# Performance work log

Measured on AMD Instinct MI355X. Metric: run time of the kernel, lower is better.

## Reference

```python
import jax, jax.numpy as jnp
import numpy as np

B, T, D, H, E, O, A = 8192, 223, 7, 128, 50, 29, 9
IMPUTE_W, LABEL_W = 0.3, 1.0

def setup_inputs() -> dict:
    key = jax.random.key(0)
    ks = jax.random.split(key, 32)
    u = lambda k, shape, fan: jax.random.uniform(k, shape, jnp.float32, -1.0/np.sqrt(fan), 1.0/np.sqrt(fan))
    return {
        'values':    jax.random.normal(ks[0], (B, T, D), jnp.float32),
        'masks':     (jax.random.uniform(ks[1], (B, T, D)) < 0.8).astype(jnp.float32),
        'deltas':    jax.random.uniform(ks[2], (B, T, D), jnp.float32) * 5.0,
        'probs':     jax.nn.softmax(jax.random.normal(ks[3], (B, O), jnp.float32), axis=1),
        'ancillary': jax.random.normal(ks[4], (B, A), jnp.float32),
        'labels':    jax.random.randint(ks[5], (B,), 0, O, jnp.int32),
        'W_td_h': u(ks[6], (H, D), H),  'b_td_h': u(ks[7], (H,), H),
        'W_td_x': u(ks[8], (D, D), D),  'b_td_x': u(ks[9], (D,), D),
        'W_hist': u(ks[10], (D, H), H), 'b_hist': u(ks[11], (D,), H),
        'W_feat': u(ks[12], (D, D), D), 'b_feat': u(ks[13], (D,), D),
        'W_comb': u(ks[14], (D, 2*D), 2*D), 'b_comb': u(ks[15], (D,), 2*D),
        'W_ih': u(ks[16], (4*H, 2*D), H), 'W_hh': u(ks[17], (4*H, H), H),
        'b_ih': u(ks[18], (4*H,), H),     'b_hh': u(ks[19], (4*H,), H),
        'W_anc': u(ks[20], (E, A), A),    'b_anc': u(ks[21], (E,), A),
        'W_cat': u(ks[22], (H, H + E), H + E), 'b_cat': u(ks[23], (H,), H + E),
        'W_out': u(ks[24], (O, H), H),    'b_out': u(ks[25], (O,), H),
    }

def _rits_forward(values, masks, deltas, probs, ancillary,
                  W_td_h, b_td_h, W_td_x, b_td_x, W_hist, b_hist,
                  W_feat, b_feat, W_comb, b_comb, W_ih, W_hh, b_ih, b_hh,
                  W_anc, b_anc, W_cat, b_cat, W_out, b_out):
    Bn = values.shape[0]
    td_x_diag = jnp.diag(W_td_x)                     # diag=True decay uses only diagonal
    Wf = W_feat * (1.0 - jnp.eye(D, dtype=W_feat.dtype))

    def step(carry, xt):
        h, c, xl = carry
        x, m, d = xt                                  # each [B, D]
        gamma_h = jnp.exp(-jax.nn.relu(d @ W_td_h.T + b_td_h))   # [B, H]
        gamma_x = jnp.exp(-jax.nn.relu(d * td_x_diag + b_td_x))  # [B, D]
        h = h * gamma_h
        x_h = h @ W_hist.T + b_hist
        msum = jnp.sum(m) + 1e-5
        xl = xl + jnp.sum(jnp.abs(x - x_h) * m) / msum
        x_c = m * x + (1.0 - m) * x_h
        z_h = x_c @ Wf.T + b_feat
        xl = xl + jnp.sum(jnp.abs(x - z_h) * m) / msum
        alpha = jnp.concatenate([gamma_x, m], axis=1) @ W_comb.T + b_comb
        c_h = alpha * z_h + (1.0 - alpha) * x_h
        xl = xl + jnp.sum(jnp.abs(x - c_h) * m) / msum
        c_c = m * x + (1.0 - m) * c_h
        inputs = jnp.concatenate([c_c, m], axis=1)    # [B, 2D]
        gates = inputs @ W_ih.T + b_ih + h @ W_hh.T + b_hh  # [B, 4H]
        i, f, g, o = jnp.split(gates, 4, axis=1)
        c = jax.nn.sigmoid(f) * c + jax.nn.sigmoid(i) * jnp.tanh(g)
        h = jax.nn.sigmoid(o) * jnp.tanh(c)
        return (h, c, xl), c_c

    h0 = jnp.zeros((Bn, H), values.dtype)
    c0 = jnp.zeros((Bn, H), values.dtype)
    xs = (jnp.swapaxes(values, 0, 1), jnp.swapaxes(masks, 0, 1), jnp.swapaxes(deltas, 0, 1))
    (h, c, x_loss), imps = jax.lax.scan(step, (h0, c0, jnp.float32(0.0)), xs)
    imputations = jnp.swapaxes(imps, 0, 1)           # [B, T, D]

    x_loss = x_loss * IMPUTE_W
    anc = jax.nn.relu(ancillary @ W_anc.T + b_anc)
    h = jax.nn.relu(jnp.concatenate([h, anc], axis=1) @ W_cat.T + b_cat)
    y_h = jax.nn.softmax(h @ W_out.T + b_out, axis=1)
    y_loss = jnp.sum((y_h - probs) ** 2) / (Bn + 1e-5) * LABEL_W
    return x_loss, y_loss, x_loss + y_loss, y_h, imputations

def reference(values, masks, deltas, probs, ancillary, labels,
              W_td_h, b_td_h, W_td_x, b_td_x, W_hist, b_hist,
              W_feat, b_feat, W_comb, b_comb, W_ih, W_hh, b_ih, b_hh,
              W_anc, b_anc, W_cat, b_cat, W_out, b_out):
    x_loss, y_loss, loss, y_h, imputations = _rits_forward(
        values, masks, deltas, probs, ancillary,
        W_td_h, b_td_h, W_td_x, b_td_x, W_hist, b_hist,
        W_feat, b_feat, W_comb, b_comb, W_ih, W_hh, b_ih, b_hh,
        W_anc, b_anc, W_cat, b_cat, W_out, b_out)
    return (x_loss, y_loss, loss, y_h, imputations, labels)
```

## Files before the change

### kernel.cpp

```cpp
#include <hip/hip_runtime.h>
#include <math.h>

#define B_ 8192
#define T_ 223
#define D_ 7
#define H_ 128
#define E_ 50
#define O_ 29
#define A_ 9
#define TD_ (T_*D_)
#define NB 16
#define NTHR 512
#define MB 8
#define MS_BG 128

#define WS_MINV  0
#define WS_ACC   (WS_MINV + T_)
#define WS_WCATT (WS_ACC + 2)
#define WS_HFIN  (WS_WCATT + 178*H_)

#define OUT_YH  3
#define OUT_IMP (OUT_YH + B_*O_)
#define OUT_LAB (OUT_IMP + B_*T_*D_)

typedef __attribute__((ext_vector_type(8))) short short8;
typedef __attribute__((ext_vector_type(4))) float floatx4;
#define MFMA16(Av,Bv,Cv) __builtin_amdgcn_mfma_f32_16x16x32_bf16((Av),(Bv),(Cv),0,0,0)

#define BARRIER() do { asm volatile("s_waitcnt lgkmcnt(0)" ::: "memory"); \
                       __builtin_amdgcn_s_barrier(); } while (0)

__device__ __forceinline__ unsigned short f2bf(float f) {
    unsigned int u = __builtin_bit_cast(unsigned int, f);
    return (unsigned short)((u + 0x7FFFu + ((u >> 16) & 1u)) >> 16);
}
__device__ __forceinline__ float bf2f(unsigned short s) {
    unsigned int u = ((unsigned int)s) << 16;
    return __builtin_bit_cast(float, u);
}
__device__ __forceinline__ float rcp_(float x)  { return __builtin_amdgcn_rcpf(x); }
__device__ __forceinline__ float sigm(float x)  { return rcp_(1.f + __expf(-x)); }
__device__ __forceinline__ float tanh_(float x) { return 1.f - 2.f*rcp_(1.f + __expf(2.f*x)); }

__global__ void rits_prep(const float* __restrict__ W_cat, float* __restrict__ ws)
{
    int idx = blockIdx.x * 256 + threadIdx.x;
    if (idx < H_*178) {
        int j = idx / 178, k = idx - j*178;
        ws[WS_WCATT + k*H_ + j] = W_cat[idx];
    }
    if (idx < T_) ws[WS_MINV + idx] = 0.f;
    if (idx < 2) ws[WS_ACC + idx] = 0.f;
}

__global__ void rits_msum(const float* __restrict__ masks, float* __restrict__ ws)
{
    const int tc = blockIdx.x % 7;
    const int bg = blockIdx.x / 7;
    const int t0 = tc * 32;
    const int nt = (t0 + 32 <= T_) ? 32 : (T_ - t0);
    const int ncol = nt * D_;
    const int tid = threadIdx.x;
    __shared__ float sums[224];
    float s = 0.f;
    if (tid < ncol) {
        const int bpg = B_ / MS_BG;
        const float* p = masks + (size_t)bg * bpg * TD_ + (size_t)t0 * D_ + tid;
        #pragma unroll 4
        for (int b = 0; b < bpg; ++b) s += p[(size_t)b * TD_];
    }
    if (tid < 224) sums[tid] = (tid < ncol) ? s : 0.f;
    __syncthreads();
    if (tid < 32) {
        float r = 0.f;
        #pragma unroll
        for (int q = 0; q < 7; ++q) r += sums[tid*7 + q];
        if (t0 + tid < T_) atomicAdd(&ws[WS_MINV + t0 + tid], r);
    }
}

__global__ __launch_bounds__(NTHR, 2) void rits_main(
    const float* __restrict__ values, const float* __restrict__ masks, const float* __restrict__ deltas,
    const float* __restrict__ W_td_h, const float* __restrict__ b_td_h,
    const float* __restrict__ W_td_x, const float* __restrict__ b_td_x,
    const float* __restrict__ W_hist, const float* __restrict__ b_hist,
    const float* __restrict__ W_feat, const float* __restrict__ b_feat,
    const float* __restrict__ W_comb, const float* __restrict__ b_comb,
    const float* __restrict__ W_ih, const float* __restrict__ W_hh,
    const float* __restrict__ b_ih, const float* __restrict__ b_hh,
    float* __restrict__ ws, float* __restrict__ out)
{
    __shared__ __attribute__((aligned(16))) unsigned short hbuf[NB*168];
    __shared__ __attribute__((aligned(16))) unsigned short bbuf[NB*32];
    __shared__ __attribute__((aligned(16))) unsigned short whis_lds[16*136];
    __shared__ float xm_l[NB*18];
    __shared__ float gx_l[NB*9];
    __shared__ float xh_l[NB*10];
    __shared__ float impbuf[NB*16*7];
    __shared__ float red[8];

    const int tid  = threadIdx.x;
    const int b0   = blockIdx.x * NB;
    const int lane = tid & 63;
    const int w    = tid >> 6;
    const int quad = lane >> 4;
    const int l15  = lane & 15;

    for (int i = tid; i < NB*168; i += NTHR) hbuf[i] = 0;
    for (int i = tid; i < NB*32;  i += NTHR) bbuf[i] = 0;
    for (int i = tid; i < 16*136; i += NTHR) {
        int r = i / 136, c = i - r*136;
        whis_lds[i] = (r < 7 && c < 128) ? f2bf(W_hist[r*H_ + c]) : 0;
    }
    __syncthreads();
    if (tid < NB) {
        bbuf[tid*32 + 7]  = 0x3F80;
        bbuf[tid*32 + 15] = 0x3F80;
    }

    short8 whhf[4][4];
    short8 winf_c[4];
    short8 winf_mb[4];
    short8 wtdf;
    float  bh_r[4];
    {
        union UU { short8 v; unsigned short u[8]; } fr;
        #pragma unroll
        for (int c = 0; c < 4; ++c) {
            const int j = (c*8 + w)*16 + l15;
            #pragma unroll
            for (int s = 0; s < 4; ++s) {
                const float* p = W_hh + j*H_ + s*32 + quad*8;
                #pragma unroll
                for (int e = 0; e < 8; ++e) fr.u[e] = f2bf(p[e]);
                whhf[c][s] = fr.v;
            }
            #pragma unroll
            for (int e = 0; e < 8; ++e) {
                int k = quad*8 + e;
                fr.u[e] = (k < 7) ? f2bf(W_ih[j*14 + k]) : (unsigned short)0;
            }
            winf_c[c] = fr.v;
            #pragma unroll
            for (int e = 0; e < 8; ++e) {
                int k = quad*8 + e;
                float v = (k < 7) ? W_ih[j*14 + 7 + k]
                        : ((k == 7) ? (b_ih[j] + b_hh[j]) : 0.f);
                fr.u[e] = f2bf(v);
            }
            winf_mb[c] = fr.v;
        }
        const int j2 = w*16 + l15;
        #pragma unroll
        for (int e = 0; e < 8; ++e) {
            int k = quad*8 + e;
            float v = (k >= 8 && k < 15) ? W_td_h[j2*D_ + (k - 8)]
                    : ((k == 15) ? b_td_h[j2] : 0.f);
            fr.u[e] = f2bf(v);
        }
        wtdf = fr.v;
        #pragma unroll
        for (int r = 0; r < 4; ++r) {
            int f = quad*4 + r;
            bh_r[r] = (quad < 2 && f < 7) ? b_hist[f] : 0.f;
        }
    }

    const bool ldr = (tid < NB*D_);
    const int  lb  = tid / D_, li = tid - (tid/D_)*D_;
    float wfr[7], wcr[14], bfr = 0.f, bcr = 0.f, tdx_own = 0.f, btdx_own = 0.f;
    if (ldr) {
        #pragma unroll
        for (int k = 0; k < 7; ++k)  wfr[k] = (k == li) ? 0.f : W_feat[li*D_ + k];
        #pragma unroll
        for (int k = 0; k < 14; ++k) wcr[k] = W_comb[li*14 + k];
        bfr = b_feat[li];  bcr = b_comb[li];
        tdx_own = W_td_x[li*D_ + li];  btdx_own = b_td_x[li];
    }

    float c_st[4] = {0,0,0,0};
    float lacc = 0.f;

    const long gbase = (long)(b0 + lb)*TD_ + li;
    float rx = 0.f, rm = 0.f, rd = 0.f;
    const float* msums = ws + WS_MINV;
    float rmv = 0.f;
    if (ldr) { rx = values[gbase]; rm = masks[gbase]; rd = deltas[gbase]; rmv = msums[0]; }

    for (int t = 0; t < T_; ++t) {
        float msum_cur = rmv;
        if (ldr) {
            float2 s2 = { rx, rm };
            *(float2*)&xm_l[lb*18 + 2*li] = s2;
            gx_l[lb*9 + li] = __expf(-fmaxf(fmaf(rd, tdx_own, btdx_own), 0.f));
            bbuf[lb*32 + li] = f2bf(rm);
            if (t + 1 < T_) {
                const long g = gbase + (long)(t+1)*D_;
                rx = values[g]; rm = masks[g]; rd = deltas[g];
                rmv = msums[t+1];
            }
        }
        BARRIER();

        floatx4 acc[4];
        #pragma unroll
        for (int c = 0; c < 4; ++c) { floatx4 z = {0,0,0,0}; acc[c] = z; }
        floatx4 xh0 = {0,0,0,0};
        #pragma unroll
        for (int s = 0; s < 4; ++s) {
            short8 hb0 = *(const short8*)&hbuf[l15*168 + s*32 + quad*8];
            #pragma unroll
            for (int c = 0; c < 4; ++c)
                acc[c] = MFMA16(whhf[c][s], hb0, acc[c]);
            if (w == 7) {
                short8 wh = *(const short8*)&whis_lds[l15*136 + s*32 + quad*8];
                xh0 = MFMA16(wh, hb0, xh0);
            }
        }
        if (w == 7 && quad < 2) {
            const int b = l15;
            float2 p0 = { xh0[0] + bh_r[0], xh0[1] + bh_r[1] };
            float2 p1 = { xh0[2] + bh_r[2], xh0[3] + bh_r[3] };
            *(float2*)&xh_l[b*10 + quad*4]     = p0;
            *(float2*)&xh_l[b*10 + quad*4 + 2] = p1;
        }
        BARRIER();

        {
            short8 bb0 = *(const short8*)&bbuf[l15*32 + quad*8];
            #pragma unroll
            for (int c = 0; c < 4; ++c)
                acc[c] = MFMA16(winf_mb[c], bb0, acc[c]);
        }

        if (ldr) {
            const int b = lb, i = li;
            const float invt = rcp_(msum_cur + 1e-5f);
            const float x = xm_l[b*18 + 2*i], m = xm_l[b*18 + 2*i + 1];
            const float xhv = xh_l[b*10 + i];
            float zh = bfr, al = bcr;
            #pragma unroll
            for (int k = 0; k < 7; ++k) {
                const float xk  = xm_l[b*18 + 2*k];
                const float mk  = xm_l[b*18 + 2*k + 1];
                const float xhk = xh_l[b*10 + k];
                const float xck = mk*xk + (1.f - mk)*xhk;
                zh = fmaf(wfr[k], xck, zh);
                al = fmaf(wcr[k], gx_l[b*9 + k], al);
                al = fmaf(wcr[7+k], mk, al);
            }
            const float ch = al*zh + (1.f - al)*xhv;
            const float cc = m*x + (1.f - m)*ch;
            impbuf[(b*16 + (t & 15))*7 + i] = cc;
            hbuf[b*168 + 128 + i] = f2bf(cc);
            lacc = fmaf((fabsf(x-xhv) + fabsf(x-zh) + fabsf(x-ch)) * m, invt, lacc);
            if (t + 1 < T_)
                bbuf[lb*32 + 8 + li] = f2bf(rd);
        }
        BARRIER();

        {
            short8 ib0 = *(const short8*)&hbuf[l15*168 + 128 + quad*8];
            #pragma unroll
            for (int c = 0; c < 4; ++c)
                acc[c] = MFMA16(winf_c[c], ib0, acc[c]);
        }
        const bool dec = (t + 1 < T_);
        floatx4 g0 = {0,0,0,0};
        if (dec) {
            short8 bb0 = *(const short8*)&bbuf[l15*32 + quad*8];
            floatx4 z = {0,0,0,0};
            g0 = MFMA16(wtdf, bb0, z);
        }
        {
            const int b = l15;
            float hnv[4];
            #pragma unroll
            for (int r = 0; r < 4; ++r) {
                float ig = acc[0][r], fg = acc[1][r];
                float gv = acc[2][r], og = acc[3][r];
                float cn = sigm(fg)*c_st[r] + sigm(ig)*tanh_(gv);
                c_st[r] = cn;
                float hn = sigm(og)*tanh_(cn);
                if (dec) hn *= __expf(-fmaxf(g0[r], 0.f));
                hnv[r] = hn;
            }
            uint2 pk;
            pk.x = (unsigned)f2bf(hnv[0]) | ((unsigned)f2bf(hnv[1]) << 16);
            pk.y = (unsigned)f2bf(hnv[2]) | ((unsigned)f2bf(hnv[3]) << 16);
            *(uint2*)&hbuf[b*168 + w*16 + quad*4] = pk;
        }

        if ((t & 15) == 15 || t == T_ - 1) {
            const int t0 = t & ~15;
            const int b  = tid >> 4, c16 = tid & 15;
            if (b < NB && t0 + c16 <= t) {
                float* gp = out + (size_t)OUT_IMP + (size_t)(b0+b)*TD_ + (size_t)(t0+c16)*D_;
                const float* lp = &impbuf[(b*16 + c16)*7];
                #pragma unroll
                for (int e = 0; e < 7; ++e) gp[e] = lp[e];
            }
        }
    }
    __syncthreads();

    for (int off = 32; off > 0; off >>= 1) lacc += __shfl_down(lacc, off, 64);
    if ((tid & 63) == 0) red[tid >> 6] = lacc;
    __syncthreads();
    if (tid == 0) {
        float s = 0.f;
        #pragma unroll
        for (int q = 0; q < 8; ++q) s += red[q];
        atomicAdd(&ws[WS_ACC], s);
    }
    for (int i = tid; i < NB*H_; i += NTHR) {
        int b = i >> 7, j = i & 127;
        ws[WS_HFIN + (size_t)(b0+b)*H_ + j] = bf2f(hbuf[b*168 + j]);
    }
}

__global__ __launch_bounds__(128) void rits_head(
    const float* __restrict__ probs, const float* __restrict__ ancillary, const int* __restrict__ labels,
    const float* __restrict__ W_anc, const float* __restrict__ b_anc,
    const float* __restrict__ b_cat,
    const float* __restrict__ W_out, const float* __restrict__ b_out,
    float* __restrict__ ws, float* __restrict__ out)
{
    __shared__ float hb[MB*H_];
    __shared__ float ancl[MB*52];
    __shared__ float hc[MB*H_];
    __shared__ float lg[MB*32];
    __shared__ float smx[MB], sinv[MB], ysum[MB];
    __shared__ float sq[MB*32];
    const int tid = threadIdx.x;
    const int bb0 = blockIdx.x * MB;

    for (int i = tid; i < MB*H_; i += 128) hb[i] = ws[WS_HFIN + (size_t)bb0*H_ + i];
    for (int i = tid; i < MB*E_; i += 128) {
        int b = i / E_, e = i - b*E_;
        float s = b_anc[e];
        #pragma unroll
        for (int a = 0; a < A_; ++a) s = fmaf(ancillary[(bb0+b)*A_ + a], W_anc[e*A_ + a], s);
        ancl[b*52+e] = fmaxf(s, 0.f);
    }
    __syncthreads();
    {
        const int j = tid;
        float s[MB];
        #pragma unroll
        for (int b = 0; b < MB; ++b) s[b] = b_cat[j];
        const float* wc = ws + WS_WCATT;
        for (int k = 0; k < H_; ++k) {
            float wv = wc[k*H_ + j];
            #pragma unroll
            for (int b = 0; b < MB; ++b) s[b] = fmaf(hb[b*H_+k], wv, s[b]);
        }
        for (int k = 0; k < E_; ++k) {
            float wv = wc[(H_+k)*H_ + j];
            #pragma unroll
            for (int b = 0; b < MB; ++b) s[b] = fmaf(ancl[b*52+k], wv, s[b]);
        }
        #pragma unroll
        for (int b = 0; b < MB; ++b) hc[b*H_+j] = fmaxf(s[b], 0.f);
    }
    __syncthreads();
    for (int i = tid; i < MB*O_; i += 128) {
        int b = i / O_, o = i - b*O_;
        float s = b_out[o];
        for (int k = 0; k < H_; ++k) s = fmaf(hc[b*H_+k], W_out[o*H_+k], s);
        lg[b*32+o] = s;
    }
    __syncthreads();
    if (tid < MB) {
        float mx = -1e30f;
        for (int o = 0; o < O_; ++o) mx = fmaxf(mx, lg[tid*32+o]);
        float se = 0.f;
        for (int o = 0; o < O_; ++o) se += __expf(lg[tid*32+o] - mx);
        smx[tid] = mx; sinv[tid] = 1.f / se;
    }
    __syncthreads();
    for (int i = tid; i < MB*O_; i += 128) {
        int b = i / O_, o = i - b*O_;
        float y = __expf(lg[b*32+o] - smx[b]) * sinv[b];
        out[OUT_YH + (size_t)(bb0+b)*O_ + o] = y;
        float d = y - probs[(size_t)(bb0+b)*O_ + o];
        sq[b*32+o] = d*d;
    }
    __syncthreads();
    if (tid < MB) {
        float s = 0.f;
        for (int o = 0; o < O_; ++o) s += sq[tid*32+o];
        ysum[tid] = s;
        out[OUT_LAB + bb0 + tid] = (float)labels[bb0 + tid];
    }
    __syncthreads();
    if (tid == 0) {
        float s = 0.f;
        #pragma unroll
        for (int b = 0; b < MB; ++b) s += ysum[b];
        atomicAdd(&ws[WS_ACC+1], s);
    }
}

__global__ void rits_fin(const float* __restrict__ ws, float* __restrict__ out)
{
    if (blockIdx.x == 0 && threadIdx.x == 0) {
        float xl = ws[WS_ACC] * 0.3f;
        float yl = ws[WS_ACC+1] * (1.0f / (8192.0f + 1e-5f));
        out[0] = xl; out[1] = yl; out[2] = xl + yl;
    }
}

extern "C" void kernel_launch(void* const* d_in, const int* in_sizes, int n_in,
                              void* d_out, int out_size, void* d_ws, size_t ws_size,
                              hipStream_t stream)
{
    const float* values = (const float*)d_in[0];
    const float* masks  = (const float*)d_in[1];
    const float* deltas = (const float*)d_in[2];
    const float* probs  = (const float*)d_in[3];
    const float* ancil  = (const float*)d_in[4];
    const int*   labels = (const int*)  d_in[5];
    const float* W_td_h = (const float*)d_in[6];
    const float* b_td_h = (const float*)d_in[7];
    const float* W_td_x = (const float*)d_in[8];
    const float* b_td_x = (const float*)d_in[9];
    const float* W_hist = (const float*)d_in[10];
    const float* b_hist = (const float*)d_in[11];
    const float* W_feat = (const float*)d_in[12];
    const float* b_feat = (const float*)d_in[13];
    const float* W_comb = (const float*)d_in[14];
    const float* b_comb = (const float*)d_in[15];
    const float* W_ih   = (const float*)d_in[16];
    const float* W_hh   = (const float*)d_in[17];
    const float* b_ih   = (const float*)d_in[18];
    const float* b_hh   = (const float*)d_in[19];
    const float* W_anc  = (const float*)d_in[20];
    const float* b_anc  = (const float*)d_in[21];
    const float* W_cat  = (const float*)d_in[22];
    const float* b_cat  = (const float*)d_in[23];
    const float* W_out  = (const float*)d_in[24];
    const float* b_out  = (const float*)d_in[25];
    float* ws  = (float*)d_ws;
    float* out = (float*)d_out;

    hipLaunchKernelGGL(rits_prep, dim3((H_*178 + 255)/256), dim3(256), 0, stream, W_cat, ws);
    hipLaunchKernelGGL(rits_msum, dim3(7*MS_BG), dim3(256), 0, stream, masks, ws);
    hipLaunchKernelGGL(rits_main, dim3(B_/NB), dim3(NTHR), 0, stream,
                       values, masks, deltas, W_td_h, b_td_h, W_td_x, b_td_x,
                       W_hist, b_hist, W_feat, b_feat, W_comb, b_comb,
                       W_ih, W_hh, b_ih, b_hh, ws, out);
    hipLaunchKernelGGL(rits_head, dim3(B_/MB), dim3(128), 0, stream,
                       probs, ancil, labels, W_anc, b_anc, b_cat, W_out, b_out, ws, out);
    hipLaunchKernelGGL(rits_fin, dim3(1), dim3(1), 0, stream, ws, out);
}
```

Baseline: 1.028 ms.

## Move input/decay weights to LDS and fuse mask-bias MFMA to raise occupancy

Raises the launch-bounds occupancy hint from 2 to 4 blocks per CU. To fit the tighter register budget, the W_ih input and mask fragments, the W_td_h decay fragment, the feature/combine regression weights and the small bias vectors move from registers into LDS. The separate mask+bias MFMA is merged into the imputation MFMA by packing [cc, m, 1] into one 24-wide K slice, which removes one MFMA pass per step. The cost is extra LDS reads every step and more LDS per block, which may itself cap occupancy below the requested level.

```diff
diff --git a/kernel.cpp b/kernel.cpp
--- a/kernel.cpp
+++ b/kernel.cpp
@@ -79,7 +79,7 @@
     }
 }
 
-__global__ __launch_bounds__(NTHR, 2) void rits_main(
+__global__ __launch_bounds__(NTHR, 4) void rits_main(
     const float* __restrict__ values, const float* __restrict__ masks, const float* __restrict__ deltas,
     const float* __restrict__ W_td_h, const float* __restrict__ b_td_h,
     const float* __restrict__ W_td_x, const float* __restrict__ b_td_x,
@@ -93,6 +93,12 @@
     __shared__ __attribute__((aligned(16))) unsigned short hbuf[NB*168];
     __shared__ __attribute__((aligned(16))) unsigned short bbuf[NB*32];
     __shared__ __attribute__((aligned(16))) unsigned short whis_lds[16*136];
+    __shared__ __attribute__((aligned(16))) unsigned short wext_lds[512*24];
+    __shared__ __attribute__((aligned(16))) unsigned short wtd_lds[128*8];
+    __shared__ __attribute__((aligned(16))) unsigned short zpad[8];
+    __shared__ float wfc_l[56];
+    __shared__ float wcb_l[112];
+    __shared__ float tdx_l[8], btdx_l[8], bh_l[8];
     __shared__ float xm_l[NB*18];
     __shared__ float gx_l[NB*9];
     __shared__ float xh_l[NB*10];
@@ -112,17 +118,42 @@
         int r = i / 136, c = i - r*136;
         whis_lds[i] = (r < 7 && c < 128) ? f2bf(W_hist[r*H_ + c]) : 0;
     }
+    for (int i = tid; i < 512*24; i += NTHR) {
+        int j = i / 24, k = i - j*24;
+        float v = (k < 14) ? W_ih[j*14 + k]
+                : ((k == 14) ? (b_ih[j] + b_hh[j]) : 0.f);
+        wext_lds[i] = f2bf(v);
+    }
+    for (int i = tid; i < 128*8; i += NTHR) {
+        int j = i >> 3, k = i & 7;
+        wtd_lds[i] = f2bf((k < 7) ? W_td_h[j*D_ + k] : b_td_h[j]);
+    }
+    if (tid < 56) {
+        int i = tid >> 3, k = tid & 7;
+        wfc_l[tid] = (k < 7) ? ((k == i) ? 0.f : W_feat[i*D_ + k]) : b_feat[i];
+    }
+    if (tid >= 64 && tid < 176) {
+        int q = tid - 64; int i = q >> 4, k = q & 15;
+        float v;
+        if (k < 7)       v = W_comb[i*14 + k];
+        else if (k < 14) v = W_comb[i*14 + k];
+        else if (k == 14) v = b_comb[i];
+        else             v = 0.f;
+        wcb_l[q] = v;
+    }
+    if (tid < 8) {
+        zpad[tid]  = 0;
+        tdx_l[tid]  = (tid < 7) ? W_td_x[tid*D_ + tid] : 0.f;
+        btdx_l[tid] = (tid < 7) ? b_td_x[tid] : 0.f;
+        bh_l[tid]   = (tid < 7) ? b_hist[tid] : 0.f;
+    }
     __syncthreads();
     if (tid < NB) {
-        bbuf[tid*32 + 7]  = 0x3F80;
-        bbuf[tid*32 + 15] = 0x3F80;
+        hbuf[tid*168 + 142] = 0x3F80;
+        bbuf[tid*32 + 7]    = 0x3F80;
     }
 
     short8 whhf[4][4];
-    short8 winf_c[4];
-    short8 winf_mb[4];
-    short8 wtdf;
-    float  bh_r[4];
     {
         union UU { short8 v; unsigned short u[8]; } fr;
         #pragma unroll
@@ -135,48 +166,11 @@
                 for (int e = 0; e < 8; ++e) fr.u[e] = f2bf(p[e]);
                 whhf[c][s] = fr.v;
             }
-            #pragma unroll
-            for (int e = 0; e < 8; ++e) {
-                int k = quad*8 + e;
-                fr.u[e] = (k < 7) ? f2bf(W_ih[j*14 + k]) : (unsigned short)0;
-            }
-            winf_c[c] = fr.v;
-            #pragma unroll
-            for (int e = 0; e < 8; ++e) {
-                int k = quad*8 + e;
-                float v = (k < 7) ? W_ih[j*14 + 7 + k]
-                        : ((k == 7) ? (b_ih[j] + b_hh[j]) : 0.f);
-                fr.u[e] = f2bf(v);
-            }
-            winf_mb[c] = fr.v;
-        }
-        const int j2 = w*16 + l15;
-        #pragma unroll
-        for (int e = 0; e < 8; ++e) {
-            int k = quad*8 + e;
-            float v = (k >= 8 && k < 15) ? W_td_h[j2*D_ + (k - 8)]
-                    : ((k == 15) ? b_td_h[j2] : 0.f);
-            fr.u[e] = f2bf(v);
-        }
-        wtdf = fr.v;
-        #pragma unroll
-        for (int r = 0; r < 4; ++r) {
-            int f = quad*4 + r;
-            bh_r[r] = (quad < 2 && f < 7) ? b_hist[f] : 0.f;
         }
     }
 
     const bool ldr = (tid < NB*D_);
     const int  lb  = tid / D_, li = tid - (tid/D_)*D_;
-    float wfr[7], wcr[14], bfr = 0.f, bcr = 0.f, tdx_own = 0.f, btdx_own = 0.f;
-    if (ldr) {
-        #pragma unroll
-        for (int k = 0; k < 7; ++k)  wfr[k] = (k == li) ? 0.f : W_feat[li*D_ + k];
-        #pragma unroll
-        for (int k = 0; k < 14; ++k) wcr[k] = W_comb[li*14 + k];
-        bfr = b_feat[li];  bcr = b_comb[li];
-        tdx_own = W_td_x[li*D_ + li];  btdx_own = b_td_x[li];
-    }
 
     float c_st[4] = {0,0,0,0};
     float lacc = 0.f;
@@ -189,16 +183,17 @@
 
     for (int t = 0; t < T_; ++t) {
         float msum_cur = rmv;
+        float x_cur = rx, m_cur = rm, d_nxt;
         if (ldr) {
             float2 s2 = { rx, rm };
             *(float2*)&xm_l[lb*18 + 2*li] = s2;
-            gx_l[lb*9 + li] = __expf(-fmaxf(fmaf(rd, tdx_own, btdx_own), 0.f));
-            bbuf[lb*32 + li] = f2bf(rm);
+            gx_l[lb*9 + li] = __expf(-fmaxf(fmaf(rd, tdx_l[li], btdx_l[li]), 0.f));
             if (t + 1 < T_) {
                 const long g = gbase + (long)(t+1)*D_;
                 rx = values[g]; rm = masks[g]; rd = deltas[g];
                 rmv = msums[t+1];
             }
+            d_nxt = rd;
         }
         BARRIER();
 
@@ -219,58 +214,59 @@
         }
         if (w == 7 && quad < 2) {
             const int b = l15;
-            float2 p0 = { xh0[0] + bh_r[0], xh0[1] + bh_r[1] };
-            float2 p1 = { xh0[2] + bh_r[2], xh0[3] + bh_r[3] };
+            float2 p0 = { xh0[0] + bh_l[quad*4+0], xh0[1] + bh_l[quad*4+1] };
+            float2 p1 = { xh0[2] + bh_l[quad*4+2], xh0[3] + bh_l[quad*4+3] };
             *(float2*)&xh_l[b*10 + quad*4]     = p0;
             *(float2*)&xh_l[b*10 + quad*4 + 2] = p1;
         }
         BARRIER();
-
-        {
-            short8 bb0 = *(const short8*)&bbuf[l15*32 + quad*8];
-            #pragma unroll
-            for (int c = 0; c < 4; ++c)
-                acc[c] = MFMA16(winf_mb[c], bb0, acc[c]);
-        }
 
         if (ldr) {
             const int b = lb, i = li;
             const float invt = rcp_(msum_cur + 1e-5f);
-            const float x = xm_l[b*18 + 2*i], m = xm_l[b*18 + 2*i + 1];
+            const float x = x_cur, m = m_cur;
             const float xhv = xh_l[b*10 + i];
-            float zh = bfr, al = bcr;
+            float zh = wfc_l[i*8 + 7], al = wcb_l[i*16 + 14];
             #pragma unroll
             for (int k = 0; k < 7; ++k) {
                 const float xk  = xm_l[b*18 + 2*k];
                 const float mk  = xm_l[b*18 + 2*k + 1];
                 const float xhk = xh_l[b*10 + k];
                 const float xck = mk*xk + (1.f - mk)*xhk;
-                zh = fmaf(wfr[k], xck, zh);
-                al = fmaf(wcr[k], gx_l[b*9 + k], al);
-                al = fmaf(wcr[7+k], mk, al);
+                zh = fmaf(wfc_l[i*8 + k], xck, zh);
+                al = fmaf(wcb_l[i*16 + k], gx_l[b*9 + k], al);
+                al = fmaf(wcb_l[i*16 + 7 + k], mk, al);
             }
             const float ch = al*zh + (1.f - al)*xhv;
             const float cc = m*x + (1.f - m)*ch;
             impbuf[(b*16 + (t & 15))*7 + i] = cc;
             hbuf[b*168 + 128 + i] = f2bf(cc);
+            hbuf[b*168 + 135 + i] = f2bf(m);
             lacc = fmaf((fabsf(x-xhv) + fabsf(x-zh) + fabsf(x-ch)) * m, invt, lacc);
             if (t + 1 < T_)
-                bbuf[lb*32 + 8 + li] = f2bf(rd);
+                bbuf[lb*32 + li] = f2bf(d_nxt);
         }
         BARRIER();
 
         {
             short8 ib0 = *(const short8*)&hbuf[l15*168 + 128 + quad*8];
             #pragma unroll
-            for (int c = 0; c < 4; ++c)
-                acc[c] = MFMA16(winf_c[c], ib0, acc[c]);
+            for (int c = 0; c < 4; ++c) {
+                const unsigned short* ap = (quad < 2)
+                    ? &wext_lds[((c*8 + w)*16 + l15)*24 + quad*8] : zpad;
+                short8 af = *(const short8*)ap;
+                acc[c] = MFMA16(af, ib0, acc[c]);
+            }
         }
         const bool dec = (t + 1 < T_);
         floatx4 g0 = {0,0,0,0};
         if (dec) {
-            short8 bb0 = *(const short8*)&bbuf[l15*32 + quad*8];
+            const unsigned short* tp = (quad == 0)
+                ? &wtd_lds[(w*16 + l15)*8] : zpad;
+            short8 af = *(const short8*)tp;
+            short8 db = *(const short8*)&bbuf[l15*32 + quad*8];
             floatx4 z = {0,0,0,0};
-            g0 = MFMA16(wtdf, bb0, z);
+            g0 = MFMA16(af, db, z);
         }
         {
             const int b = l15;
```

After: 2.055 ms. 2x slower.
